# Performance work log

Measured on AMD Instinct MI355X. Metric: run time of the kernel, lower is better.

The kernel has to match this reference:

```python
import jax, jax.numpy as jnp
import numpy as np

# dims
B = 16        # batch
S = 32        # question seq len
H = 768       # bert-base hidden
E = 200000    # num entities
T = 200000    # padded triples per example
R = 500       # num relations
STEPS = 3     # num_steps
WAYS = 2      # num_ways


def setup_inputs() -> dict:
    key = jax.random.key(0)
    ks = jax.random.split(key, 10)
    # one-hot head entity per example (start distribution)
    head_ids = jax.random.randint(ks[0], (B,), 0, E)
    heads = jnp.zeros((B, E), jnp.float32).at[jnp.arange(B), head_ids].set(1.0)
    q_embeddings = jax.random.normal(ks[1], (B, H), jnp.float32)
    q_word_h = jax.random.normal(ks[2], (B, S, H), jnp.float32)
    attention_mask = jnp.ones((B, S), jnp.float32)
    # padded per-example triples (sub, rel, obj)
    sub = jax.random.randint(ks[3], (B, T), 0, E)
    rel = jax.random.randint(ks[4], (B, T), 0, R)
    obj = jax.random.randint(ks[5], (B, T), 0, E)
    triples = jnp.stack([sub, rel, obj], axis=-1).astype(jnp.int32)  # [B,T,3]
    scale = 0.02
    step_W = jax.random.normal(ks[6], (WAYS, STEPS, H, H), jnp.float32) * scale
    step_b = jnp.zeros((WAYS, STEPS, H), jnp.float32)
    rel_W = jax.random.normal(ks[7], (WAYS, H, R), jnp.float32) * scale
    rel_b = jnp.zeros((WAYS, R), jnp.float32)
    hop_W = jax.random.normal(ks[8], (WAYS, H, STEPS), jnp.float32) * scale
    hop_b = jnp.zeros((WAYS, STEPS), jnp.float32)
    return dict(heads=heads, q_embeddings=q_embeddings, q_word_h=q_word_h,
                attention_mask=attention_mask, step_W=step_W, step_b=step_b,
                rel_W=rel_W, rel_b=rel_b, hop_W=hop_W, hop_b=hop_b,
                triples=triples)


def _propagate(last_e, triples, rel_dist):
    # last_e: [E], triples: [T,3], rel_dist: [R] -> [E]
    sub, rel, obj = triples[:, 0], triples[:, 1], triples[:, 2]
    obj_p = last_e[sub] * rel_dist[rel]                 # gather + gate  [T]
    return jax.ops.segment_sum(obj_p, obj, num_segments=E)  # scatter-add [E]


def reference(heads, q_embeddings, q_word_h, attention_mask,
              step_W, step_b, rel_W, rel_b, hop_W, hop_b, triples):
    e_score = []
    for w in range(WAYS):
        last_e = heads                                   # [B,E]
        ent_probs = []
        for t in range(STEPS):
            cq_t = jnp.tanh(q_embeddings @ step_W[w, t] + step_b[w, t])   # [B,H]
            q_logits = jnp.einsum('bh,bsh->bs', cq_t, q_word_h)            # [B,S]
            q_dist = jax.nn.softmax(q_logits, axis=1) * attention_mask
            q_dist = q_dist / (jnp.sum(q_dist, axis=1, keepdims=True) + 1e-6)
            ctx_h = jnp.einsum('bs,bsh->bh', q_dist, q_word_h)             # [B,H]
            rel_dist = jax.nn.sigmoid(ctx_h @ rel_W[w] + rel_b[w])         # [B,R]
            last_e = jax.vmap(_propagate)(last_e, triples, rel_dist)      # [B,E]
            # renormalize entries > 1 (detached divisor, as in original)
            z = jax.lax.stop_gradient(jnp.where(last_e > 1.0, last_e, 1.0))
            last_e = last_e / z
            ent_probs.append(last_e)
        hop_res = jnp.stack(ent_probs, axis=1)                             # [B,STEPS,E]
        hop_attn = jax.nn.softmax(q_embeddings @ hop_W[w] + hop_b[w], axis=1)  # [B,STEPS]
        e_score.append(jnp.einsum('bse,bs->be', hop_res, hop_attn))
    return jnp.prod(jnp.stack(e_score), axis=0)                            # [B,E]
```

## Files before the change

### kernel.cpp

```cpp
#include <hip/hip_runtime.h>
#include <math.h>

#define NB 16
#define NS 32
#define NH 768
#define NE 200000
#define NT 200000
#define NR 500
#define NSTEPS 3
#define NWAYS 2

#define HSZ 2048
#define AHSZ 4096
#define BMW 6272
#define PCHUNK 25

typedef unsigned int u32;

__device__ __forceinline__ int fhash(int e) { return (int)(((u32)e * 2654435761u) >> 21); }
__device__ __forceinline__ int ahash(int e) { return (int)(((u32)e * 2654435761u) >> 20); }

__global__ __launch_bounds__(256) void cq_part_kernel(
    const float* __restrict__ qe, const float* __restrict__ stepW,
    float* __restrict__ part)
{
    int blk = blockIdx.x;
    int jc = blk % 12;
    int wt = (blk / 12) % 6;
    int kc = blk / 72;

    __shared__ float s_w[192][68];
    __shared__ float s_q[NB][196];

    int tid = threadIdx.x;
    int lane = tid & 63, wv = tid >> 6;

    {
        const float* Wbase = stepW + (size_t)wt * NH * NH + (size_t)(kc * 192) * NH + jc * 64;
#pragma unroll
        for (int u = 0; u < 12; ++u) {
            int f = tid + u * 256;
            int hh = f >> 4, c4 = (f & 15) * 4;
            float4 v = *(const float4*)(Wbase + (size_t)hh * NH + c4);
            *(float4*)&s_w[hh][c4] = v;
        }
    }
    {
#pragma unroll
        for (int u = 0; u < 3; ++u) {
            int f = tid + u * 256;
            int b = f / 48, c4 = (f % 48) * 4;
            float4 v = *(const float4*)(qe + (size_t)b * NH + kc * 192 + c4);
            *(float4*)&s_q[b][c4] = v;
        }
    }
    __syncthreads();

    float acc[4] = {0.f, 0.f, 0.f, 0.f};
#pragma unroll 4
    for (int h4 = 0; h4 < 48; ++h4) {
        float w0 = s_w[h4 * 4 + 0][lane];
        float w1 = s_w[h4 * 4 + 1][lane];
        float w2 = s_w[h4 * 4 + 2][lane];
        float w3 = s_w[h4 * 4 + 3][lane];
#pragma unroll
        for (int i = 0; i < 4; ++i) {
            float4 q = *(const float4*)&s_q[wv * 4 + i][h4 * 4];
            acc[i] += w0 * q.x + w1 * q.y + w2 * q.z + w3 * q.w;
        }
    }
#pragma unroll
    for (int i = 0; i < 4; ++i) {
        int b = wv * 4 + i;
        part[(((size_t)kc * 6 + wt) * NB + b) * NH + jc * 64 + lane] = acc[i];
    }
}

__global__ __launch_bounds__(512) void qwr_kernel(
    const float* __restrict__ qwh, const float* __restrict__ relW,
    float* __restrict__ qwr)
{
    int rc = blockIdx.x & 7;
    int b  = (blockIdx.x >> 3) & 15;
    int w  = blockIdx.x >> 7;

    __shared__ float s_w[128][68];
    __shared__ float s_q[NS][132];

    int tid = threadIdx.x;
    int lane = tid & 63, wv = tid >> 6;
    int col = rc * 64 + lane;

    float acc[4] = {0.f, 0.f, 0.f, 0.f};

    for (int k0 = 0; k0 < NH; k0 += 128) {
        {
            const float* Wbase = relW + (size_t)w * NH * NR + (size_t)k0 * NR;
#pragma unroll
            for (int u = 0; u < 4; ++u) {
                int f = tid + u * 512;
                int hh = f >> 4;
                int c = rc * 64 + (f & 15) * 4;
                if (c > NR - 4) c = NR - 4;
                float4 v = *(const float4*)(Wbase + (size_t)hh * NR + c);
                *(float4*)&s_w[hh][(f & 15) * 4] = v;
            }
        }
        {
#pragma unroll
            for (int u = 0; u < 2; ++u) {
                int f = tid + u * 512;
                int s = f >> 5, c4 = (f & 31) * 4;
                float4 v = *(const float4*)(qwh + ((size_t)b * NS + s) * NH + k0 + c4);
                *(float4*)&s_q[s][c4] = v;
            }
        }
        __syncthreads();

#pragma unroll 4
        for (int h4 = 0; h4 < 32; ++h4) {
            float w0 = s_w[h4 * 4 + 0][lane];
            float w1 = s_w[h4 * 4 + 1][lane];
            float w2 = s_w[h4 * 4 + 2][lane];
            float w3 = s_w[h4 * 4 + 3][lane];
#pragma unroll
            for (int i = 0; i < 4; ++i) {
                float4 q = *(const float4*)&s_q[wv * 4 + i][h4 * 4];
                acc[i] += w0 * q.x + w1 * q.y + w2 * q.z + w3 * q.w;
            }
        }
        __syncthreads();
    }

    if (col < NR) {
#pragma unroll
        for (int i = 0; i < 4; ++i)
            qwr[(((size_t)(w * NB + b)) * NS + (wv * 4 + i)) * NR + col] = acc[i];
    }
}

__global__ __launch_bounds__(256) void attn_rel_kernel(
    const float* __restrict__ part, const float* __restrict__ stepB,
    const float* __restrict__ qwh, const float* __restrict__ mask,
    const float* __restrict__ qwr, const float* __restrict__ relB,
    const float* __restrict__ qe, const float* __restrict__ hopW,
    const float* __restrict__ hopB,
    float* __restrict__ rel, float* __restrict__ hop)
{
    int b = blockIdx.x % NB;
    int wt = blockIdx.x / NB;
    int w = wt / NSTEPS;
    int t = wt % NSTEPS;

    __shared__ float s_cq[NH];
    __shared__ float s_sm[NS];
    __shared__ float s_hl[4];

    int tid = threadIdx.x;

    for (int j = tid; j < NH; j += 256) {
        float a = stepB[wt * NH + j];
#pragma unroll
        for (int kc = 0; kc < 4; ++kc)
            a += part[(((size_t)kc * 6 + wt) * NB + b) * NH + j];
        s_cq[j] = tanhf(a);
    }
    __syncthreads();

    {
        int s = tid >> 3, l = tid & 7;
        const float* row = qwh + ((size_t)b * NS + s) * NH;
        float a = 0.f;
        for (int h = l; h < NH; h += 8) a += s_cq[h] * row[h];
        a += __shfl_down(a, 4, 8);
        a += __shfl_down(a, 2, 8);
        a += __shfl_down(a, 1, 8);
        if (l == 0) s_sm[s] = a;
    }
    __syncthreads();

    if (tid < 64) {
        float lg = (tid < 32) ? s_sm[tid] : -1e30f;
        float m = lg;
        for (int off = 16; off; off >>= 1) m = fmaxf(m, __shfl_xor(m, off, 32));
        float ev = expf(lg - m);
        float sum = ev;
        for (int off = 16; off; off >>= 1) sum += __shfl_xor(sum, off, 32);
        float d = ev / sum * ((tid < 32) ? mask[b * NS + tid] : 0.f);
        float sum2 = d;
        for (int off = 16; off; off >>= 1) sum2 += __shfl_xor(sum2, off, 32);
        d = d / (sum2 + 1e-6f);
        if (tid < 32) s_sm[tid] = d;
    }
    __syncthreads();

    {
        const float* Q = qwr + ((size_t)(w * NB + b)) * NS * NR;
        for (int r = tid; r < NR; r += 256) {
            float a = relB[w * NR + r];
#pragma unroll 8
            for (int s = 0; s < NS; ++s) a += s_sm[s] * Q[(size_t)s * NR + r];
            rel[((size_t)wt * NB + b) * NR + r] = 1.f / (1.f + expf(-a));
        }
    }

    if (t == 0) {
        int lane = tid & 63, wv = tid >> 6;
        if (wv < 3) {
            float a = 0.f;
            for (int h = lane; h < NH; h += 64)
                a += qe[b * NH + h] * hopW[((size_t)w * NH + h) * NSTEPS + wv];
            for (int off = 32; off; off >>= 1) a += __shfl_down(a, off, 64);
            if (lane == 0) s_hl[wv] = a + hopB[w * NSTEPS + wv];
        }
        __syncthreads();
        if (tid == 0) {
            float mx = fmaxf(s_hl[0], fmaxf(s_hl[1], s_hl[2]));
            float e0 = expf(s_hl[0] - mx), e1 = expf(s_hl[1] - mx), e2 = expf(s_hl[2] - mx);
            float inv = 1.f / (e0 + e1 + e2);
            hop[(w * NB + b) * NSTEPS + 0] = e0 * inv;
            hop[(w * NB + b) * NSTEPS + 1] = e1 * inv;
            hop[(w * NB + b) * NSTEPS + 2] = e2 * inv;
        }
    }
}

__global__ void head_kernel(const float* __restrict__ heads, int* __restrict__ keys0,
                            float* __restrict__ vals0, u32* __restrict__ bm0)
{
    size_t N4 = (size_t)NB * NE / 4;
    const float4* h4 = (const float4*)heads;
    for (size_t i = (size_t)blockIdx.x * blockDim.x + threadIdx.x; i < N4;
         i += (size_t)gridDim.x * blockDim.x) {
        float4 v = h4[i];
        float c[4] = { v.x, v.y, v.z, v.w };
#pragma unroll
        for (int k = 0; k < 4; ++k) {
            if (c[k] != 0.0f) {
                size_t idx = i * 4 + k;
                int b = (int)(idx / NE);
                int e = (int)(idx % NE);
                int s = fhash(e);
                keys0[(size_t)b * HSZ + s] = e + 1;
                vals0[(size_t)b * HSZ + s] = 1.0f;
                vals0[(size_t)(NB + b) * HSZ + s] = 1.0f;
                atomicOr(&bm0[(size_t)b * BMW + (e >> 5)], 1u << (e & 31));
            }
        }
    }
}

__global__ __launch_bounds__(256) void prop_kernel(
    const int* __restrict__ triples,
    const u32* __restrict__ bmIn, const int* __restrict__ keysIn, const float* __restrict__ valsIn,
    u32* __restrict__ bmOut, int* __restrict__ keysOut, float* __restrict__ valsOut,
    const float* __restrict__ rel, int t)
{
    __shared__ u32 s_bm[BMW];
    int b = blockIdx.x / PCHUNK;
    int c = blockIdx.x % PCHUNK;
    const u32* g = bmIn + (size_t)b * BMW;
    for (int k = threadIdx.x; k < BMW; k += 256) s_bm[k] = g[k];
    __syncthreads();

    const int*   kin  = keysIn  + (size_t)b * HSZ;
    const float* v0in = valsIn  + (size_t)b * HSZ;
    const float* v1in = valsIn  + (size_t)(NB + b) * HSZ;
    const float* r0 = rel + ((size_t)(0 * NSTEPS + t) * NB + b) * NR;
    const float* r1 = rel + ((size_t)(1 * NSTEPS + t) * NB + b) * NR;
    int*   kout  = keysOut + (size_t)b * HSZ;
    float* v0out = valsOut + (size_t)b * HSZ;
    float* v1out = valsOut + (size_t)(NB + b) * HSZ;
    u32*   bmo   = bmOut + (size_t)b * BMW;

    const int4* tp = (const int4*)(triples + (size_t)b * NT * 3);
    const int QPC = (NT / 4) / PCHUNK;
    int qend = (c + 1) * QPC;
    for (int q = c * QPC + threadIdx.x; q < qend; q += 256) {
        int4 x = tp[q * 3 + 0];
        int4 y = tp[q * 3 + 1];
        int4 z = tp[q * 3 + 2];
        int su[4] = { x.x, x.w, y.z, z.y };
        int re[4] = { x.y, y.x, y.w, z.z };
        int ob[4] = { x.z, y.y, z.x, z.w };
#pragma unroll
        for (int k = 0; k < 4; ++k) {
            int sub = su[k];
            if ((s_bm[sub >> 5] >> (sub & 31)) & 1u) {
                int s = fhash(sub);
                float v0 = 0.f, v1 = 0.f;
                bool found = false;
                for (int p = 0; p < HSZ; ++p) {
                    int kk = kin[s];
                    if (kk == 0) break;
                    if (kk == sub + 1) {
                        v0 = fminf(v0in[s], 1.0f);
                        v1 = fminf(v1in[s], 1.0f);
                        found = true;
                        break;
                    }
                    s = (s + 1) & (HSZ - 1);
                }
                if (found) {
                    float c0 = v0 * r0[re[k]];
                    float c1 = v1 * r1[re[k]];
                    int e = ob[k];
                    int s2 = fhash(e);
                    for (int p = 0; p < HSZ; ++p) {
                        int old = atomicCAS(&kout[s2], 0, e + 1);
                        if (old == 0 || old == e + 1) {
                            atomicAdd(&v0out[s2], c0);
                            atomicAdd(&v1out[s2], c1);
                            if (old == 0) atomicOr(&bmo[e >> 5], 1u << (e & 31));
                            break;
                        }
                        s2 = (s2 + 1) & (HSZ - 1);
                    }
                }
            }
        }
    }
}

__global__ __launch_bounds__(256) void final_kernel(
    const int* __restrict__ keysG, const float* __restrict__ valsG,
    const float* __restrict__ hop, float* __restrict__ out)
{
    __shared__ int s_k[AHSZ];
    __shared__ float s_v0[AHSZ];
    __shared__ float s_v1[AHSZ];
    int b = blockIdx.x;
    for (int i = threadIdx.x; i < AHSZ; i += 256) { s_k[i] = 0; s_v0[i] = 0.f; s_v1[i] = 0.f; }
    __syncthreads();
    for (int gen = 1; gen <= 3; ++gen) {
        const int* kg = keysG + ((size_t)gen * NB + b) * HSZ;
        const float* vg = valsG + (size_t)gen * NWAYS * NB * HSZ;
        const float* v0 = vg + (size_t)b * HSZ;
        const float* v1 = vg + (size_t)(NB + b) * HSZ;
        float h0 = hop[(0 * NB + b) * NSTEPS + (gen - 1)];
        float h1 = hop[(1 * NB + b) * NSTEPS + (gen - 1)];
        for (int i = threadIdx.x; i < HSZ; i += 256) {
            int key = kg[i];
            if (key == 0) continue;
            float a0 = h0 * fminf(v0[i], 1.0f);
            float a1 = h1 * fminf(v1[i], 1.0f);
            int s = ahash(key - 1);
            for (int p = 0; p < AHSZ; ++p) {
                int old = atomicCAS(&s_k[s], 0, key);
                if (old == 0 || old == key) {
                    atomicAdd(&s_v0[s], a0);
                    atomicAdd(&s_v1[s], a1);
                    break;
                }
                s = (s + 1) & (AHSZ - 1);
            }
        }
    }
    __syncthreads();
    for (int i = threadIdx.x; i < AHSZ; i += 256) {
        int key = s_k[i];
        if (key) out[(size_t)b * NE + (key - 1)] = s_v0[i] * s_v1[i];
    }
}

extern "C" void kernel_launch(void* const* d_in, const int* in_sizes, int n_in,
                              void* d_out, int out_size, void* d_ws, size_t ws_size,
                              hipStream_t stream)
{
    const float* heads  = (const float*)d_in[0];
    const float* qe     = (const float*)d_in[1];
    const float* qwh    = (const float*)d_in[2];
    const float* mask   = (const float*)d_in[3];
    const float* stepW  = (const float*)d_in[4];
    const float* stepB  = (const float*)d_in[5];
    const float* relW   = (const float*)d_in[6];
    const float* relB   = (const float*)d_in[7];
    const float* hopW   = (const float*)d_in[8];
    const float* hopB   = (const float*)d_in[9];
    const int*   triples = (const int*)d_in[10];
    float* out = (float*)d_out;

    int*   keysG = (int*)d_ws;
    float* valsG = (float*)(keysG + 4 * NB * HSZ);
    u32*   bmG   = (u32*)(valsG + 4 * NWAYS * NB * HSZ);
    float* rel   = (float*)(bmG + 4 * (size_t)NB * BMW);
    float* hop   = rel + (size_t)NWAYS * NSTEPS * NB * NR;
    float* part  = hop + NWAYS * NB * NSTEPS;
    float* qwr   = part + (size_t)4 * 6 * NB * NH;

    size_t zero_bytes = (char*)rel - (char*)d_ws;
    hipMemsetAsync(d_ws, 0, zero_bytes, stream);
    hipMemsetAsync(d_out, 0, (size_t)NB * NE * sizeof(float), stream);

    cq_part_kernel<<<288, 256, 0, stream>>>(qe, stepW, part);
    qwr_kernel<<<256, 512, 0, stream>>>(qwh, relW, qwr);
    head_kernel<<<2048, 256, 0, stream>>>(heads, keysG, valsG, bmG);
    attn_rel_kernel<<<96, 256, 0, stream>>>(part, stepB, qwh, mask, qwr, relB,
                                            qe, hopW, hopB, rel, hop);

    for (int t = 0; t < NSTEPS; ++t) {
        prop_kernel<<<NB * PCHUNK, 256, 0, stream>>>(
            triples,
            bmG + (size_t)t * NB * BMW,
            keysG + (size_t)t * NB * HSZ,
            valsG + (size_t)t * NWAYS * NB * HSZ,
            bmG + (size_t)(t + 1) * NB * BMW,
            keysG + (size_t)(t + 1) * NB * HSZ,
            valsG + (size_t)(t + 1) * NWAYS * NB * HSZ,
            rel, t);
    }

    final_kernel<<<NB, 256, 0, stream>>>(keysG, valsG, hop, out);
}
```

Baseline: 224.5 us.

## Reorder relation projection: compute context vectors first, then split-K matmul with relW

The old path projected every question word through relW (qwr: B*S*R outputs) before attention. The new path computes the attention-weighted context first, then multiplies the [6*16, 768] contexts by relW with a split-K kernel and a separate reduce-plus-sigmoid kernel. Per the reference maths this cuts the projection FLOPs roughly by the sequence length. It also moves the hop softmax into its own kernel and raises the propagation chunk count from 25 to 40 blocks per example. The cost is three extra kernel launches and a serial dependency on attention before the relation projection.

```diff
diff --git a/kernel.cpp b/kernel.cpp
--- a/kernel.cpp
+++ b/kernel.cpp
@@ -13,7 +13,7 @@
 #define HSZ 2048
 #define AHSZ 4096
 #define BMW 6272
-#define PCHUNK 25
+#define PCHUNK 40
 
 typedef unsigned int u32;
 
@@ -76,85 +76,16 @@
     }
 }
 
-__global__ __launch_bounds__(512) void qwr_kernel(
-    const float* __restrict__ qwh, const float* __restrict__ relW,
-    float* __restrict__ qwr)
-{
-    int rc = blockIdx.x & 7;
-    int b  = (blockIdx.x >> 3) & 15;
-    int w  = blockIdx.x >> 7;
-
-    __shared__ float s_w[128][68];
-    __shared__ float s_q[NS][132];
-
-    int tid = threadIdx.x;
-    int lane = tid & 63, wv = tid >> 6;
-    int col = rc * 64 + lane;
-
-    float acc[4] = {0.f, 0.f, 0.f, 0.f};
-
-    for (int k0 = 0; k0 < NH; k0 += 128) {
-        {
-            const float* Wbase = relW + (size_t)w * NH * NR + (size_t)k0 * NR;
-#pragma unroll
-            for (int u = 0; u < 4; ++u) {
-                int f = tid + u * 512;
-                int hh = f >> 4;
-                int c = rc * 64 + (f & 15) * 4;
-                if (c > NR - 4) c = NR - 4;
-                float4 v = *(const float4*)(Wbase + (size_t)hh * NR + c);
-                *(float4*)&s_w[hh][(f & 15) * 4] = v;
-            }
-        }
-        {
-#pragma unroll
-            for (int u = 0; u < 2; ++u) {
-                int f = tid + u * 512;
-                int s = f >> 5, c4 = (f & 31) * 4;
-                float4 v = *(const float4*)(qwh + ((size_t)b * NS + s) * NH + k0 + c4);
-                *(float4*)&s_q[s][c4] = v;
-            }
-        }
-        __syncthreads();
-
-#pragma unroll 4
-        for (int h4 = 0; h4 < 32; ++h4) {
-            float w0 = s_w[h4 * 4 + 0][lane];
-            float w1 = s_w[h4 * 4 + 1][lane];
-            float w2 = s_w[h4 * 4 + 2][lane];
-            float w3 = s_w[h4 * 4 + 3][lane];
-#pragma unroll
-            for (int i = 0; i < 4; ++i) {
-                float4 q = *(const float4*)&s_q[wv * 4 + i][h4 * 4];
-                acc[i] += w0 * q.x + w1 * q.y + w2 * q.z + w3 * q.w;
-            }
-        }
-        __syncthreads();
-    }
-
-    if (col < NR) {
-#pragma unroll
-        for (int i = 0; i < 4; ++i)
-            qwr[(((size_t)(w * NB + b)) * NS + (wv * 4 + i)) * NR + col] = acc[i];
-    }
-}
-
-__global__ __launch_bounds__(256) void attn_rel_kernel(
+__global__ __launch_bounds__(256) void attn_kernel(
     const float* __restrict__ part, const float* __restrict__ stepB,
     const float* __restrict__ qwh, const float* __restrict__ mask,
-    const float* __restrict__ qwr, const float* __restrict__ relB,
-    const float* __restrict__ qe, const float* __restrict__ hopW,
-    const float* __restrict__ hopB,
-    float* __restrict__ rel, float* __restrict__ hop)
+    float* __restrict__ ctx)
 {
     int b = blockIdx.x % NB;
     int wt = blockIdx.x / NB;
-    int w = wt / NSTEPS;
-    int t = wt % NSTEPS;
 
     __shared__ float s_cq[NH];
     __shared__ float s_sm[NS];
-    __shared__ float s_hl[4];
 
     int tid = threadIdx.x;
 
@@ -194,34 +125,105 @@
     }
     __syncthreads();
 
-    {
-        const float* Q = qwr + ((size_t)(w * NB + b)) * NS * NR;
-        for (int r = tid; r < NR; r += 256) {
-            float a = relB[w * NR + r];
+    for (int h = tid; h < NH; h += 256) {
+        const float* col = qwh + (size_t)b * NS * NH + h;
+        float c = 0.f;
 #pragma unroll 8
-            for (int s = 0; s < NS; ++s) a += s_sm[s] * Q[(size_t)s * NR + r];
-            rel[((size_t)wt * NB + b) * NR + r] = 1.f / (1.f + expf(-a));
-        }
-    }
-
-    if (t == 0) {
-        int lane = tid & 63, wv = tid >> 6;
-        if (wv < 3) {
-            float a = 0.f;
-            for (int h = lane; h < NH; h += 64)
-                a += qe[b * NH + h] * hopW[((size_t)w * NH + h) * NSTEPS + wv];
-            for (int off = 32; off; off >>= 1) a += __shfl_down(a, off, 64);
-            if (lane == 0) s_hl[wv] = a + hopB[w * NSTEPS + wv];
-        }
-        __syncthreads();
-        if (tid == 0) {
-            float mx = fmaxf(s_hl[0], fmaxf(s_hl[1], s_hl[2]));
-            float e0 = expf(s_hl[0] - mx), e1 = expf(s_hl[1] - mx), e2 = expf(s_hl[2] - mx);
-            float inv = 1.f / (e0 + e1 + e2);
-            hop[(w * NB + b) * NSTEPS + 0] = e0 * inv;
-            hop[(w * NB + b) * NSTEPS + 1] = e1 * inv;
-            hop[(w * NB + b) * NSTEPS + 2] = e2 * inv;
-        }
+        for (int s = 0; s < NS; ++s) c += s_sm[s] * col[s * NH];
+        ctx[((size_t)wt * NB + b) * NH + h] = c;
+    }
+}
+
+__global__ __launch_bounds__(256) void rel_part_kernel(
+    const float* __restrict__ ctx, const float* __restrict__ relW,
+    float* __restrict__ part_r)
+{
+    int blk = blockIdx.x;
+    int rc = blk & 7;
+    int w  = (blk >> 3) & 1;
+    int kc = blk >> 4;
+
+    __shared__ float s_ctx[48][68];
+
+    int tid = threadIdx.x;
+    int lane = tid & 63, wv = tid >> 6;
+
+#pragma unroll
+    for (int u = 0; u < 3; ++u) {
+        int f = tid + u * 256;
+        int tb = f >> 4, c4 = (f & 15) * 4;
+        int t = tb >> 4, b = tb & 15;
+        float4 v = *(const float4*)(ctx + ((size_t)(w * 3 + t) * NB + b) * NH + kc * 64 + c4);
+        *(float4*)&s_ctx[tb][c4] = v;
+    }
+    __syncthreads();
+
+    int col = rc * 64 + lane;
+    int colc = col < NR ? col : NR - 1;
+    const float* Wb = relW + (size_t)w * NH * NR + (size_t)(kc * 64) * NR + colc;
+
+    float acc[12];
+#pragma unroll
+    for (int i = 0; i < 12; ++i) acc[i] = 0.f;
+
+#pragma unroll 4
+    for (int h4 = 0; h4 < 16; ++h4) {
+        float w0 = Wb[(size_t)(h4 * 4 + 0) * NR];
+        float w1 = Wb[(size_t)(h4 * 4 + 1) * NR];
+        float w2 = Wb[(size_t)(h4 * 4 + 2) * NR];
+        float w3 = Wb[(size_t)(h4 * 4 + 3) * NR];
+#pragma unroll
+        for (int i = 0; i < 12; ++i) {
+            float4 c = *(const float4*)&s_ctx[wv * 12 + i][h4 * 4];
+            acc[i] += w0 * c.x + w1 * c.y + w2 * c.z + w3 * c.w;
+        }
+    }
+    if (col < NR) {
+#pragma unroll
+        for (int i = 0; i < 12; ++i) {
+            int tb = wv * 12 + i;
+            int t = tb >> 4, b = tb & 15;
+            part_r[(((size_t)kc * 6 + (w * 3 + t)) * NB + b) * NR + col] = acc[i];
+        }
+    }
+}
+
+__global__ void rel_reduce_kernel(const float* __restrict__ part_r,
+                                  const float* __restrict__ relB,
+                                  float* __restrict__ rel)
+{
+    int b = blockIdx.x % NB;
+    int wt = blockIdx.x / NB;
+    int w = wt / NSTEPS;
+    for (int r = threadIdx.x; r < NR; r += 256) {
+        float a = relB[w * NR + r];
+#pragma unroll
+        for (int kc = 0; kc < 12; ++kc)
+            a += part_r[(((size_t)kc * 6 + wt) * NB + b) * NR + r];
+        rel[((size_t)wt * NB + b) * NR + r] = 1.f / (1.f + expf(-a));
+    }
+}
+
+__global__ __launch_bounds__(192) void hop_kernel(
+    const float* __restrict__ qe, const float* __restrict__ hopW,
+    const float* __restrict__ hopB, float* __restrict__ hop)
+{
+    int wb = blockIdx.x;
+    int w = wb / NB, b = wb % NB;
+    int t = threadIdx.x / 64, l = threadIdx.x % 64;
+    __shared__ float s_logit[4];
+    float a = 0.f;
+    for (int h = l; h < NH; h += 64) a += qe[b * NH + h] * hopW[((size_t)w * NH + h) * NSTEPS + t];
+    for (int off = 32; off; off >>= 1) a += __shfl_down(a, off, 64);
+    if (l == 0) s_logit[t] = a + hopB[w * NSTEPS + t];
+    __syncthreads();
+    if (threadIdx.x == 0) {
+        float mx = fmaxf(s_logit[0], fmaxf(s_logit[1], s_logit[2]));
+        float e0 = expf(s_logit[0] - mx), e1 = expf(s_logit[1] - mx), e2 = expf(s_logit[2] - mx);
+        float inv = 1.f / (e0 + e1 + e2);
+        hop[wb * NSTEPS + 0] = e0 * inv;
+        hop[wb * NSTEPS + 1] = e1 * inv;
+        hop[wb * NSTEPS + 2] = e2 * inv;
     }
 }
 
@@ -386,17 +388,19 @@
     float* rel   = (float*)(bmG + 4 * (size_t)NB * BMW);
     float* hop   = rel + (size_t)NWAYS * NSTEPS * NB * NR;
     float* part  = hop + NWAYS * NB * NSTEPS;
-    float* qwr   = part + (size_t)4 * 6 * NB * NH;
+    float* ctx   = part + (size_t)4 * 6 * NB * NH;
+    float* part_r = ctx + (size_t)6 * NB * NH;
 
     size_t zero_bytes = (char*)rel - (char*)d_ws;
     hipMemsetAsync(d_ws, 0, zero_bytes, stream);
     hipMemsetAsync(d_out, 0, (size_t)NB * NE * sizeof(float), stream);
 
     cq_part_kernel<<<288, 256, 0, stream>>>(qe, stepW, part);
-    qwr_kernel<<<256, 512, 0, stream>>>(qwh, relW, qwr);
+    hop_kernel<<<NWAYS * NB, 192, 0, stream>>>(qe, hopW, hopB, hop);
     head_kernel<<<2048, 256, 0, stream>>>(heads, keysG, valsG, bmG);
-    attn_rel_kernel<<<96, 256, 0, stream>>>(part, stepB, qwh, mask, qwr, relB,
-                                            qe, hopW, hopB, rel, hop);
+    attn_kernel<<<96, 256, 0, stream>>>(part, stepB, qwh, mask, ctx);
+    rel_part_kernel<<<192, 256, 0, stream>>>(ctx, relW, part_r);
+    rel_reduce_kernel<<<96, 256, 0, stream>>>(part_r, relB, rel);
 
     for (int t = 0; t < NSTEPS; ++t) {
         prop_kernel<<<NB * PCHUNK, 256, 0, stream>>>(
```

Result: faster. 211.4 us (-5.8%).
